# Optimization experiments

Hardware: AMD Instinct MI355X
Metric: run time of the kernel (lower is better)

The kernel has to match this reference:

```python
import jax, jax.numpy as jnp
import numpy as np

LENGTH = 5
TOP_K = 5
POOL_SIZE = 60
EMBED_DIM = 768
MAP_SCALE = 0.1
MAX_NORM = 1.0 - 4e-3  # Poincare ball projection eps for float32 (geoopt convention)
EPS = 1e-12


def _l2_normalize(x):
    ss = jnp.sum(x * x, axis=-1, keepdims=True)
    return x * jax.lax.rsqrt(jnp.maximum(ss, EPS))


def _expmap0(u):
    # c = 1: expmap0(u) = tanh(||u||) * u / ||u||
    n = jnp.sqrt(jnp.maximum(jnp.sum(u * u, axis=-1, keepdims=True), 1e-15))
    return jnp.tanh(n) * u / n


def _proju0(x):
    # project onto the open unit ball
    n = jnp.sqrt(jnp.maximum(jnp.sum(x * x, axis=-1, keepdims=True), 1e-15))
    return jnp.where(n > MAX_NORM, x * (MAX_NORM / n), x)


def _map_to_ball(x):
    return _proju0(_expmap0(_l2_normalize(x) * MAP_SCALE))


def _mobius_add(x, y):
    # c = 1 Mobius addition, broadcasting over leading dims
    x2 = jnp.sum(x * x, axis=-1, keepdims=True)
    y2 = jnp.sum(y * y, axis=-1, keepdims=True)
    xy = jnp.sum(x * y, axis=-1, keepdims=True)
    num = (1.0 + 2.0 * xy + y2) * x + (1.0 - x2) * y
    den = 1.0 + 2.0 * xy + x2 * y2
    return num / jnp.maximum(den, 1e-15)


def _poincare_dist(x, y):
    # dist(x, y) = 2 * artanh(||(-x) mobius+ y||)  (c = 1)
    d = _mobius_add(-x, y)
    n = jnp.sqrt(jnp.maximum(jnp.sum(d * d, axis=-1), 1e-15))
    n = jnp.clip(n, 0.0, 1.0 - 1e-7)
    return 2.0 * jnp.arctanh(n)


def setup_inputs() -> dict:
    key = jax.random.key(0)
    k1, k2, k3 = jax.random.split(key, 3)
    x_embed = jax.random.normal(k1, (128, 512, EMBED_DIM), dtype=jnp.float32)
    prompt = jax.random.uniform(k2, (POOL_SIZE, LENGTH, EMBED_DIM), dtype=jnp.float32, minval=-1.0, maxval=1.0)
    prompt_key = jax.random.uniform(k3, (POOL_SIZE, EMBED_DIM), dtype=jnp.float32, minval=-1.0, maxval=1.0)
    return {"x_embed": x_embed, "prompt": prompt, "prompt_key": prompt_key}


def reference(x_embed, prompt, prompt_key):
    B = x_embed.shape[0]
    x_mean = jnp.mean(x_embed, axis=1)                      # [B, D]
    key_ball = _map_to_ball(prompt_key)                     # [P, D]
    q_ball = _map_to_ball(x_mean)                           # [B, D]
    dist = _poincare_dist(q_ball[:, None, :], key_ball[None, :, :])  # [B, P]
    similarity = -dist
    _, idx = jax.lax.top_k(similarity, TOP_K)               # [B, K]
    idx = jnp.sort(idx, axis=1)
    batched_prompt = prompt[idx].reshape(B, TOP_K * LENGTH, EMBED_DIM)
    selected_key = key_ball[idx]                            # [B, K, D]
    selected_dist = jnp.take_along_axis(dist, idx, axis=1)  # [B, K]
    reduce_sim = jnp.sum(selected_dist) / B
    prompted_embedding = jnp.concatenate([batched_prompt, x_embed], axis=1)
    return (prompted_embedding, reduce_sim, idx, similarity, selected_key)
```

## Files before the change

kernel.cpp:

```cpp
#include <hip/hip_runtime.h>

#define EMBED   768
#define EMBED4  192
#define POOL    60
#define BATCH   128
#define SEQ     512
#define TOPK    5
#define LEN     5
#define OUTROWS 537
#define NSLICE  16

#define SZ_PE   (128L*537L*768L)
#define OFF_RS  (SZ_PE)
#define OFF_IDX (OFF_RS + 1)
#define OFF_SIM (OFF_IDX + 640)
#define OFF_SK  (OFF_SIM + 7680)

#define WS_PARTIAL 0
#define WS_KEYBALL 1572864
#define WS_KEYY2   1618944
#define WS_SEL     1619008

#define MAX_NORM_F 0.996f

typedef float fx4 __attribute__((ext_vector_type(4)));

__device__ __forceinline__ float block_reduce_256(float v, float* red) {
    int tid = threadIdx.x;
    #pragma unroll
    for (int m = 32; m >= 1; m >>= 1) v += __shfl_xor(v, m, 64);
    if ((tid & 63) == 0) red[tid >> 6] = v;
    __syncthreads();
    float total = red[0] + red[1] + red[2] + red[3];
    __syncthreads();
    return total;
}

__global__ __launch_bounds__(192) void mean_partial_copy(
        const float* __restrict__ x, float* __restrict__ out, float* __restrict__ partial) {
    const int slice = blockIdx.x, b = blockIdx.y, tid = threadIdx.x;
    const fx4* __restrict__ x4 = (const fx4*)x;
    fx4* __restrict__ out4 = (fx4*)out;
    fx4* __restrict__ p4 = (fx4*)partial;

    if (slice == 0 && b == 0 && tid == 0) out[OFF_RS] = 0.0f;

    fx4 acc = (fx4)(0.f);
    const int rows = SEQ / NSLICE;
    const long ibase = ((long)b * SEQ + slice * rows) * EMBED4 + tid;
    const long obase = ((long)b * OUTROWS + 25 + slice * rows) * EMBED4 + tid;
    #pragma unroll
    for (int s0 = 0; s0 < rows; s0 += 8) {
        fx4 v[8];
        #pragma unroll
        for (int i = 0; i < 8; ++i)
            v[i] = __builtin_nontemporal_load(&x4[ibase + (long)(s0 + i) * EMBED4]);
        #pragma unroll
        for (int i = 0; i < 8; ++i) {
            acc += v[i];
            __builtin_nontemporal_store(v[i], &out4[obase + (long)(s0 + i) * EMBED4]);
        }
    }
    p4[(long)(b * NSLICE + slice) * EMBED4 + tid] = acc;
}

__global__ __launch_bounds__(256) void keyball_kernel(
        const float* __restrict__ pkey, float* __restrict__ keyball, float* __restrict__ keyy2) {
    __shared__ float red[4];
    const int p = blockIdx.x, tid = threadIdx.x;
    float v[3];
    float ss = 0.f;
    #pragma unroll
    for (int j = 0; j < 3; ++j) { v[j] = pkey[p * EMBED + tid + 256 * j]; ss += v[j] * v[j]; }
    ss = block_reduce_256(ss, red);
    const float scale1 = rsqrtf(fmaxf(ss, 1e-12f)) * 0.1f;
    float su = 0.f;
    #pragma unroll
    for (int j = 0; j < 3; ++j) { v[j] *= scale1; su += v[j] * v[j]; }
    su = block_reduce_256(su, red);
    const float n = sqrtf(fmaxf(su, 1e-15f));
    const float f = tanhf(n) / n;
    float sb = 0.f;
    #pragma unroll
    for (int j = 0; j < 3; ++j) { v[j] *= f; sb += v[j] * v[j]; }
    sb = block_reduce_256(sb, red);
    const float n2 = sqrtf(fmaxf(sb, 1e-15f));
    const float g = (n2 > MAX_NORM_F) ? (MAX_NORM_F / n2) : 1.0f;
    #pragma unroll
    for (int j = 0; j < 3; ++j) keyball[p * EMBED + tid + 256 * j] = v[j] * g;
    if (tid == 0) keyy2[p] = sb * g * g;
}

__global__ __launch_bounds__(256) void topk_core(
        const float* __restrict__ partial, const float* __restrict__ keyball,
        const float* __restrict__ keyy2, float* __restrict__ out, int* __restrict__ selw) {
    __shared__ float red[4];
    __shared__ float q[EMBED];
    __shared__ float xy[POOL];
    __shared__ float dist[POOL];
    const int b = blockIdx.x, tid = threadIdx.x;

    float v[3];
    {
        const float inv = 1.0f / (float)SEQ;
        #pragma unroll
        for (int j = 0; j < 3; ++j) {
            const int col = tid + 256 * j;
            float s = 0.f;
            #pragma unroll
            for (int sl = 0; sl < NSLICE; ++sl)
                s += partial[(long)(b * NSLICE + sl) * EMBED + col];
            v[j] = s * inv;
        }
    }

    float ss = 0.f;
    #pragma unroll
    for (int j = 0; j < 3; ++j) ss += v[j] * v[j];
    ss = block_reduce_256(ss, red);
    const float scale1 = rsqrtf(fmaxf(ss, 1e-12f)) * 0.1f;
    float su = 0.f;
    #pragma unroll
    for (int j = 0; j < 3; ++j) { v[j] *= scale1; su += v[j] * v[j]; }
    su = block_reduce_256(su, red);
    const float n = sqrtf(fmaxf(su, 1e-15f));
    const float f = tanhf(n) / n;
    float sb = 0.f;
    #pragma unroll
    for (int j = 0; j < 3; ++j) { v[j] *= f; sb += v[j] * v[j]; }
    sb = block_reduce_256(sb, red);
    const float n2 = sqrtf(fmaxf(sb, 1e-15f));
    const float g = (n2 > MAX_NORM_F) ? (MAX_NORM_F / n2) : 1.0f;
    const float x2 = sb * g * g;
    #pragma unroll
    for (int j = 0; j < 3; ++j) q[tid + 256 * j] = v[j] * g;
    __syncthreads();

    const int wave = tid >> 6, lane = tid & 63;
    for (int p = wave; p < POOL; p += 4) {
        const float* __restrict__ kb = keyball + p * EMBED;
        float acc = 0.f;
        #pragma unroll
        for (int d = 0; d < EMBED; d += 64) acc += q[d + lane] * kb[d + lane];
        #pragma unroll
        for (int m = 32; m >= 1; m >>= 1) acc += __shfl_xor(acc, m, 64);
        if (lane == 0) xy[p] = acc;
    }
    __syncthreads();

    if (tid < POOL) {
        const float s = xy[tid];
        const float y2 = keyy2[tid];
        const float A = 1.0f - 2.0f * s + y2;
        const float B = 1.0f - x2;
        const float num2 = A * A * x2 + B * B * y2 - 2.0f * A * B * s;
        const float den = fmaxf(1.0f - 2.0f * s + x2 * y2, 1e-15f);
        float nn = sqrtf(fmaxf(num2 / (den * den), 1e-15f));
        nn = fminf(fmaxf(nn, 0.0f), 1.0f - 1e-7f);
        const float dd = logf((1.0f + nn) / (1.0f - nn));
        dist[tid] = dd;
        out[OFF_SIM + (long)b * POOL + tid] = -dd;
    }
    __syncthreads();

    if (tid == 0) {
        int sel[TOPK];
        unsigned long long mask = 0ULL;
        for (int k = 0; k < TOPK; ++k) {
            int best = 0; float bd = 1e30f;
            for (int p = 0; p < POOL; ++p) {
                if (mask & (1ULL << p)) continue;
                if (dist[p] < bd) { bd = dist[p]; best = p; }
            }
            mask |= 1ULL << best;
            sel[k] = best;
        }
        #pragma unroll
        for (int i = 0; i < TOPK; ++i)
            for (int j2 = i + 1; j2 < TOPK; ++j2)
                if (sel[j2] < sel[i]) { int t = sel[i]; sel[i] = sel[j2]; sel[j2] = t; }
        float sum = 0.f;
        for (int k = 0; k < TOPK; ++k) {
            sum += dist[sel[k]];
            out[OFF_IDX + (long)b * TOPK + k] = (float)sel[k];
            selw[b * TOPK + k] = sel[k];
        }
        atomicAdd(&out[OFF_RS], sum * (1.0f / 128.0f));
    }
}

__global__ __launch_bounds__(192) void gather_kernel(
        const float* __restrict__ prompt, const float* __restrict__ keyball,
        const int* __restrict__ selw, float* __restrict__ out) {
    const int r = blockIdx.x, b = blockIdx.y, tid = threadIdx.x;
    if (r < TOPK * LEN) {
        const int k = r / LEN, l = r - k * LEN;
        const int pi = selw[b * TOPK + k];
        const float4* __restrict__ src = (const float4*)prompt + ((long)pi * LEN + l) * EMBED4;
        float4* __restrict__ dst = (float4*)out + ((long)b * OUTROWS + r) * EMBED4;
        dst[tid] = src[tid];
    } else {
        const int k = r - TOPK * LEN;
        const int pi = selw[b * TOPK + k];
        const float* __restrict__ src = keyball + (long)pi * EMBED;
        float* __restrict__ dst = out + OFF_SK + ((long)b * TOPK + k) * EMBED;
        #pragma unroll
        for (int j = 0; j < 4; ++j) dst[tid + 192 * j] = src[tid + 192 * j];
    }
}

extern "C" void kernel_launch(void* const* d_in, const int* in_sizes, int n_in,
                              void* d_out, int out_size, void* d_ws, size_t ws_size,
                              hipStream_t stream) {
    const float* x      = (const float*)d_in[0];
    const float* prompt = (const float*)d_in[1];
    const float* pkey   = (const float*)d_in[2];
    float* out = (float*)d_out;
    float* ws  = (float*)d_ws;

    float* partial = ws + WS_PARTIAL;
    float* keyball = ws + WS_KEYBALL;
    float* keyy2   = ws + WS_KEYY2;
    int*   selw    = (int*)(ws + WS_SEL);

    hipLaunchKernelGGL(mean_partial_copy, dim3(NSLICE, 128), dim3(192), 0, stream, x, out, partial);
    hipLaunchKernelGGL(keyball_kernel,    dim3(60),          dim3(256), 0, stream, pkey, keyball, keyy2);
    hipLaunchKernelGGL(topk_core,         dim3(128),         dim3(256), 0, stream,
                       partial, keyball, keyy2, out, selw);
    hipLaunchKernelGGL(gather_kernel,     dim3(30, 128),     dim3(192), 0, stream,
                       prompt, keyball, selw, out);
}
```

Baseline: 377.6 us.

## Widen copy unroll, dual-row dot products, and wave-parallel top-k selection

The mean/copy kernel now loads 16 rows per batch instead of 8, so more memory requests are in flight. In topk_core, query values are held in registers and each wave computes two key dot products per iteration. The serial single-thread top-k scan becomes a wave-wide shuffle argmin repeated five times, with ties broken by lower index. Together these aim to cut latency in the small top-k kernel and raise memory-level parallelism in the dominant copy, at the cost of more register use.

Result: faster. 363.1 us (-3.8%).

```diff
diff --git a/kernel.cpp b/kernel.cpp
--- a/kernel.cpp
+++ b/kernel.cpp
@@ -50,13 +50,13 @@
     const long ibase = ((long)b * SEQ + slice * rows) * EMBED4 + tid;
     const long obase = ((long)b * OUTROWS + 25 + slice * rows) * EMBED4 + tid;
     #pragma unroll
-    for (int s0 = 0; s0 < rows; s0 += 8) {
-        fx4 v[8];
-        #pragma unroll
-        for (int i = 0; i < 8; ++i)
+    for (int s0 = 0; s0 < rows; s0 += 16) {
+        fx4 v[16];
+        #pragma unroll
+        for (int i = 0; i < 16; ++i)
             v[i] = __builtin_nontemporal_load(&x4[ibase + (long)(s0 + i) * EMBED4]);
         #pragma unroll
-        for (int i = 0; i < 8; ++i) {
+        for (int i = 0; i < 16; ++i) {
             acc += v[i];
             __builtin_nontemporal_store(v[i], &out4[obase + (long)(s0 + i) * EMBED4]);
         }
@@ -137,14 +137,31 @@
     __syncthreads();
 
     const int wave = tid >> 6, lane = tid & 63;
-    for (int p = wave; p < POOL; p += 4) {
-        const float* __restrict__ kb = keyball + p * EMBED;
-        float acc = 0.f;
-        #pragma unroll
-        for (int d = 0; d < EMBED; d += 64) acc += q[d + lane] * kb[d + lane];
-        #pragma unroll
-        for (int m = 32; m >= 1; m >>= 1) acc += __shfl_xor(acc, m, 64);
-        if (lane == 0) xy[p] = acc;
+    {
+        float qv[12];
+        #pragma unroll
+        for (int j = 0; j < 12; ++j) qv[j] = q[j * 64 + lane];
+        for (int p = wave; p < POOL; p += 8) {
+            const int p2 = p + 4;
+            const bool has2 = (p2 < POOL);
+            const float* __restrict__ kb1 = keyball + (long)p * EMBED;
+            const float* __restrict__ kb2 = keyball + (long)(has2 ? p2 : p) * EMBED;
+            float acc1 = 0.f, acc2 = 0.f;
+            #pragma unroll
+            for (int j = 0; j < 12; ++j) {
+                acc1 += qv[j] * kb1[j * 64 + lane];
+                acc2 += qv[j] * kb2[j * 64 + lane];
+            }
+            #pragma unroll
+            for (int m = 32; m >= 1; m >>= 1) {
+                acc1 += __shfl_xor(acc1, m, 64);
+                acc2 += __shfl_xor(acc2, m, 64);
+            }
+            if (lane == 0) {
+                xy[p] = acc1;
+                if (has2) xy[p2] = acc2;
+            }
+        }
     }
     __syncthreads();
 
@@ -163,29 +180,35 @@
     }
     __syncthreads();
 
-    if (tid == 0) {
+    if (wave == 0) {
+        float myd = (lane < POOL) ? dist[lane] : 1e30f;
+        const int myi = lane;
         int sel[TOPK];
-        unsigned long long mask = 0ULL;
+        #pragma unroll
         for (int k = 0; k < TOPK; ++k) {
-            int best = 0; float bd = 1e30f;
-            for (int p = 0; p < POOL; ++p) {
-                if (mask & (1ULL << p)) continue;
-                if (dist[p] < bd) { bd = dist[p]; best = p; }
-            }
-            mask |= 1ULL << best;
-            sel[k] = best;
-        }
-        #pragma unroll
-        for (int i = 0; i < TOPK; ++i)
-            for (int j2 = i + 1; j2 < TOPK; ++j2)
-                if (sel[j2] < sel[i]) { int t = sel[i]; sel[i] = sel[j2]; sel[j2] = t; }
-        float sum = 0.f;
-        for (int k = 0; k < TOPK; ++k) {
-            sum += dist[sel[k]];
-            out[OFF_IDX + (long)b * TOPK + k] = (float)sel[k];
-            selw[b * TOPK + k] = sel[k];
-        }
-        atomicAdd(&out[OFF_RS], sum * (1.0f / 128.0f));
+            float bd = myd; int bi = myi;
+            #pragma unroll
+            for (int m = 32; m >= 1; m >>= 1) {
+                const float od = __shfl_xor(bd, m, 64);
+                const int   oi = __shfl_xor(bi, m, 64);
+                if (od < bd || (od == bd && oi < bi)) { bd = od; bi = oi; }
+            }
+            sel[k] = bi;
+            if (myi == bi) myd = 1e30f;
+        }
+        if (lane == 0) {
+            #pragma unroll
+            for (int i = 0; i < TOPK; ++i)
+                for (int j2 = i + 1; j2 < TOPK; ++j2)
+                    if (sel[j2] < sel[i]) { int t = sel[i]; sel[i] = sel[j2]; sel[j2] = t; }
+            float sum = 0.f;
+            for (int k = 0; k < TOPK; ++k) {
+                sum += dist[sel[k]];
+                out[OFF_IDX + (long)b * TOPK + k] = (float)sel[k];
+                selw[b * TOPK + k] = sel[k];
+            }
+            atomicAdd(&out[OFF_RS], sum * (1.0f / 128.0f));
+        }
     }
 }
 
```
